# Optimization experiments

Hardware: AMD Instinct MI355X
Metric: run time of the kernel (lower is better)

## Reference

```python
import jax, jax.numpy as jnp
import numpy as np

NUM_REF = 20
LINE_SCORE_THRESH = 0.6
MIN_PLANE_AREA = 100
H, W, N_LINES = 480, 640, 100


def _sobel(x):
    # x: [B,1,H,W] -> [B,2,H,W]; standard Sobel edge conv (kx, ky), padding=1
    kx = jnp.array([[1., 0., -1.], [2., 0., -2.], [1., 0., -1.]], x.dtype)
    ky = jnp.array([[1., 2., 1.], [0., 0., 0.], [-1., -2., -1.]], x.dtype)
    k = jnp.stack([kx, ky])[:, None]  # [2,1,3,3]
    return jax.lax.conv_general_dilated(x, k, (1, 1), [(1, 1), (1, 1)],
                                         dimension_numbers=('NCHW', 'OIHW', 'NCHW'))


def setup_inputs() -> dict:
    key = jax.random.key(0)
    k1, k2, k3, k4, k5 = jax.random.split(key, 5)
    depth_pred = jax.random.normal(k1, (1, 1, H, W), jnp.float32)
    depth_gt = jax.random.uniform(k2, (1, 1, H, W), jnp.float32)
    line_pred = jax.random.uniform(k3, (1, N_LINES, 6), jnp.float32)
    line_score = jax.random.normal(k4, (1, N_LINES, 2), jnp.float32)
    valid_mask = jax.random.randint(k5, (1, 1, H, W), 0, 2) > 0
    return {"depth_pred": depth_pred, "depth_gt": depth_gt,
            "line_pred": line_pred, "line_score": line_score,
            "valid_mask": valid_mask}


def reference(depth_pred, depth_gt, line_pred, line_score, valid_mask):
    h, w = depth_pred.shape[-2:]
    # how many lines pass the softmax threshold -> number of planes actually used
    probs = jax.nn.softmax(line_score, axis=-1)
    num_kept = jnp.sum(probs[0, :, 0] > LINE_SCORE_THRESH)
    top_num = jnp.minimum(num_kept, NUM_REF)
    # top-k by raw class-0 logit (torch.topk is sorted, so top `top_num` = prefix)
    _, t_ids = jax.lax.top_k(line_score[0, :, 0], NUM_REF)
    chosen = line_pred[0][t_ids]  # [P,6]
    scale = jnp.array([w, h, w, h, w, h], jnp.float32)
    xy = jnp.round(chosen * scale).reshape(NUM_REF, 3, 2)  # [P,3,(x,y)]
    xy = jnp.stack([jnp.clip(xy[..., 0], 0, w - 1),
                    jnp.clip(xy[..., 1], 0, h - 1)], axis=-1)
    # Sobel normal map
    g = _sobel(depth_pred)              # [1,2,H,W]
    nx, ny = -g[0, 0], -g[0, 1]          # [H,W]
    valid = valid_mask[0, 0]             # [H,W] bool
    # vectorized point-in-triangle: cross-product sign test for all P planes
    px = jnp.arange(w, dtype=jnp.float32).reshape(1, 1, 1, w)
    py = jnp.arange(h, dtype=jnp.float32).reshape(1, 1, h, 1)
    nxt = xy[:, jnp.array([1, 2, 0])]
    ex = (nxt[..., 0] - xy[..., 0])[..., None, None]  # [P,3,1,1]
    ey = (nxt[..., 1] - xy[..., 1])[..., None, None]
    vx = xy[..., 0][..., None, None]
    vy = xy[..., 1][..., None, None]
    d = ex * (py - vy) - ey * (px - vx)               # [P,3,H,W]
    inside = jnp.all(d >= 0, axis=1) | jnp.all(d <= 0, axis=1)  # [P,H,W]
    m = inside & valid
    cnt = jnp.sum(m, axis=(1, 2)).astype(jnp.float32)  # [P]
    safe = jnp.maximum(cnt, 1.0)
    mf = m.astype(nx.dtype)
    mean_x = jnp.sum(mf * nx, axis=(1, 2)) / safe
    mean_y = jnp.sum(mf * ny, axis=(1, 2)) / safe
    var_x = jnp.sum(mf * (nx - mean_x[:, None, None]) ** 2, axis=(1, 2)) / safe
    var_y = jnp.sum(mf * (ny - mean_y[:, None, None]) ** 2, axis=(1, 2)) / safe
    include = (cnt >= MIN_PLANE_AREA) & (jnp.arange(NUM_REF) < top_num)
    total = jnp.maximum(jnp.sum(include), 1).astype(jnp.float32)
    loss_var = jnp.sum(jnp.where(include, var_x + var_y, 0.0)) / total
    return loss_var
```

## Files before the change

### kernel.cpp

```cpp
#include <hip/hip_runtime.h>
#include <math.h>

#define HH 480
#define WW 640
#define NL 100
#define NREF 20
#define RPB 2
#define NB (HH / RPB)


__global__ __launch_bounds__(256) void plane_main_kernel(
    const float* __restrict__ depth, const int* __restrict__ valid,
    const float* __restrict__ line_pred, const float* __restrict__ line_score,
    float* __restrict__ w) {
    __shared__ float ds[(RPB + 2) * WW];
    __shared__ int vsh[RPB * WW];
    __shared__ float s_sc[NL];
    __shared__ float s_vert[NREF][6];
    __shared__ float s_ae[RPB][NREF * 3];
    __shared__ float s_ey[NREF * 3];

    const int tid = threadIdx.x;
    const int base = blockIdx.x * RPB;

    if (tid < NL) s_sc[tid] = ((const float2*)line_score)[tid].x;

    for (int idx = tid; idx < (RPB + 2) * (WW / 4); idx += 256) {
        const int lr = idx / (WW / 4);
        const int c4 = idx - lr * (WW / 4);
        const int g = base - 1 + lr;
        float4 v = make_float4(0.f, 0.f, 0.f, 0.f);
        if ((unsigned)g < (unsigned)HH) v = ((const float4*)depth)[g * (WW / 4) + c4];
        ((float4*)ds)[idx] = v;
    }
    for (int idx = tid; idx < RPB * (WW / 4); idx += 256)
        ((int4*)vsh)[idx] = ((const int4*)valid)[base * (WW / 4) + idx];
    __syncthreads();

    if (tid < NL) {
        const float s0 = s_sc[tid];
        int rank = 0;
        for (int j = 0; j < NL; j++) {
            const float sj = s_sc[j];
            rank += ((sj > s0) || (sj == s0 && j < tid)) ? 1 : 0;
        }
        if (rank < NREF) {
            const float2 c01 = ((const float2*)line_pred)[3 * tid];
            const float2 c23 = ((const float2*)line_pred)[3 * tid + 1];
            const float2 c45 = ((const float2*)line_pred)[3 * tid + 2];
            s_vert[rank][0] = fminf(fmaxf(rintf(c01.x * (float)WW), 0.f), (float)(WW - 1));
            s_vert[rank][1] = fminf(fmaxf(rintf(c01.y * (float)HH), 0.f), (float)(HH - 1));
            s_vert[rank][2] = fminf(fmaxf(rintf(c23.x * (float)WW), 0.f), (float)(WW - 1));
            s_vert[rank][3] = fminf(fmaxf(rintf(c23.y * (float)HH), 0.f), (float)(HH - 1));
            s_vert[rank][4] = fminf(fmaxf(rintf(c45.x * (float)WW), 0.f), (float)(WW - 1));
            s_vert[rank][5] = fminf(fmaxf(rintf(c45.y * (float)HH), 0.f), (float)(HH - 1));
        }
    }
    __syncthreads();

    if (tid < NREF * 3) {
        const int t = tid / 3, e = tid - 3 * t, n = (e + 1) % 3;
        const float vx = s_vert[t][2 * e], vy = s_vert[t][2 * e + 1];
        const float ex = s_vert[t][2 * n] - vx, eyv = s_vert[t][2 * n + 1] - vy;
        s_ey[tid] = eyv;
        #pragma unroll
        for (int rr = 0; rr < RPB; rr++)
            s_ae[rr][tid] = fmaf(ex, (float)(base + rr) - vy, eyv * vx);
    }
    __syncthreads();

    const int wid = tid >> 6, lane = tid & 63;
    float eyr[5][3];
    #pragma unroll
    for (int i = 0; i < 5; i++)
        #pragma unroll
        for (int e = 0; e < 3; e++)
            eyr[i][e] = s_ey[(wid * 5 + i) * 3 + e];

    float acc[5][4];
    #pragma unroll
    for (int i = 0; i < 5; i++)
        #pragma unroll
        for (int q = 0; q < 4; q++) acc[i][q] = 0.f;

    #pragma unroll
    for (int rr = 0; rr < RPB; rr++) {
        float ae[5][3];
        #pragma unroll
        for (int i = 0; i < 5; i++)
            #pragma unroll
            for (int e = 0; e < 3; e++)
                ae[i][e] = s_ae[rr][(wid * 5 + i) * 3 + e];
        const float* rm = ds + rr * WW;
        const float* rc = ds + (rr + 1) * WW;
        const float* rp = ds + (rr + 2) * WW;
        const int* vrow = vsh + rr * WW;
        #pragma unroll
        for (int j = 0; j < 10; j++) {
            const int x = j * 64 + lane;
            const float px = (float)x;
            const float fl = (x > 0) ? 1.f : 0.f;
            const float fr = (x < WW - 1) ? 1.f : 0.f;
            const int xm = x - (x > 0), xp = x + (x < WW - 1);
            const float a00 = rm[xm] * fl, a01 = rm[x], a02 = rm[xp] * fr;
            const float a10 = rc[xm] * fl,               a12 = rc[xp] * fr;
            const float a20 = rp[xm] * fl, a21 = rp[x], a22 = rp[xp] * fr;
            const float gx = (a00 - a02) + 2.f * (a10 - a12) + (a20 - a22);
            const float gy = (a00 + 2.f * a01 + a02) - (a20 + 2.f * a21 + a22);
            const float nx = -gx, ny = -gy;
            const float s2 = nx * nx + ny * ny;
            const bool vm = (vrow[x] != 0);
            #pragma unroll
            for (int i = 0; i < 5; i++) {
                const float d0 = fmaf(-eyr[i][0], px, ae[i][0]);
                const float d1 = fmaf(-eyr[i][1], px, ae[i][1]);
                const float d2 = fmaf(-eyr[i][2], px, ae[i][2]);
                const float dmin = fminf(fminf(d0, d1), d2);
                const float dmax = fmaxf(fmaxf(d0, d1), d2);
                const bool m = ((dmin >= 0.f) | (dmax <= 0.f)) & vm;
                const float mf = m ? 1.f : 0.f;
                acc[i][0] += mf;
                acc[i][1] = fmaf(mf, nx, acc[i][1]);
                acc[i][2] = fmaf(mf, ny, acc[i][2]);
                acc[i][3] = fmaf(mf, s2, acc[i][3]);
            }
        }
    }

    #pragma unroll
    for (int off = 32; off > 0; off >>= 1)
        #pragma unroll
        for (int i = 0; i < 5; i++)
            #pragma unroll
            for (int q = 0; q < 4; q++)
                acc[i][q] += __shfl_down(acc[i][q], off);
    if (lane == 0) {
        #pragma unroll
        for (int i = 0; i < 5; i++)
            #pragma unroll
            for (int q = 0; q < 4; q++)
                w[((wid * 5 + i) * 4 + q) * NB + blockIdx.x] = acc[i][q];
    }
}

__global__ __launch_bounds__(128) void plane_finalize_kernel(
    const float* __restrict__ line_score, const float* __restrict__ w,
    float* __restrict__ out) {
    __shared__ float s_col[NREF * 4];
    __shared__ int s_cnt[2];
    const int tid = threadIdx.x;
    const int lane = tid & 63, wid = tid >> 6;

    int flag = 0;
    if (tid < NL) {
        const float2 sc = ((const float2*)line_score)[tid];
        const float p0 = 1.0f / (1.0f + expf(sc.y - sc.x));
        flag = (p0 > 0.6f) ? 1 : 0;
    }
    const unsigned long long b = __ballot(flag);
    if (lane == 0) s_cnt[wid] = __popcll(b);

    if (tid < NREF * 4) {
        const float4* col = (const float4*)(w + tid * NB);
        float4 s4 = make_float4(0.f, 0.f, 0.f, 0.f);
        #pragma unroll 4
        for (int p = 0; p < NB / 4; p++) {
            const float4 v = col[p];
            s4.x += v.x; s4.y += v.y; s4.z += v.z; s4.w += v.w;
        }
        s_col[tid] = (s4.x + s4.y) + (s4.z + s4.w);
    }
    __syncthreads();

    const int topnum = min(s_cnt[0] + s_cnt[1], NREF);
    float val = 0.f, inc = 0.f;
    if (tid < NREF) {
        const float c  = s_col[tid * 4 + 0];
        const float sx = s_col[tid * 4 + 1];
        const float sy = s_col[tid * 4 + 2];
        const float sq = s_col[tid * 4 + 3];
        const float safe = fmaxf(c, 1.f);
        const float mx = sx / safe, my = sy / safe;
        const float var = (sq - 2.f * mx * sx - 2.f * my * sy
                           + c * (mx * mx + my * my)) / safe;
        inc = ((c >= 100.f) && (tid < topnum)) ? 1.f : 0.f;
        val = inc * var;
    }
    if (tid < 64) {
        #pragma unroll
        for (int off = 32; off > 0; off >>= 1) {
            val += __shfl_down(val, off);
            inc += __shfl_down(inc, off);
        }
        if (tid == 0) out[0] = val / fmaxf(inc, 1.f);
    }
}

extern "C" void kernel_launch(void* const* d_in, const int* in_sizes, int n_in,
                              void* d_out, int out_size, void* d_ws, size_t ws_size,
                              hipStream_t stream) {
    const float* depth_pred = (const float*)d_in[0];
    const float* line_pred  = (const float*)d_in[2];
    const float* line_score = (const float*)d_in[3];
    const int*   valid_mask = (const int*)d_in[4];
    float* out = (float*)d_out;
    float* w = (float*)d_ws;

    plane_main_kernel<<<NB, 256, 0, stream>>>(depth_pred, valid_mask,
                                              line_pred, line_score, w);
    plane_finalize_kernel<<<1, 128, 0, stream>>>(line_score, w, out);
}
```

Baseline: 78.24 us.

## Fuse finalize into main kernel via last-block atomic ticket

```diff
diff --git a/kernel.cpp b/kernel.cpp
--- a/kernel.cpp
+++ b/kernel.cpp
@@ -9,16 +9,19 @@
 #define NB (HH / RPB)
 
 
-__global__ __launch_bounds__(256) void plane_main_kernel(
+__global__ __launch_bounds__(256) void plane_fused_kernel(
     const float* __restrict__ depth, const int* __restrict__ valid,
     const float* __restrict__ line_pred, const float* __restrict__ line_score,
-    float* __restrict__ w) {
+    float* __restrict__ w, float* __restrict__ out) {
     __shared__ float ds[(RPB + 2) * WW];
     __shared__ int vsh[RPB * WW];
     __shared__ float s_sc[NL];
     __shared__ float s_vert[NREF][6];
     __shared__ float s_ae[RPB][NREF * 3];
     __shared__ float s_ey[NREF * 3];
+    __shared__ float s_col[NREF * 4];
+    __shared__ int s_cnt[2];
+    __shared__ int s_last;
 
     const int tid = threadIdx.x;
     const int base = blockIdx.x * RPB;
@@ -134,22 +137,27 @@
             #pragma unroll
             for (int q = 0; q < 4; q++)
                 acc[i][q] += __shfl_down(acc[i][q], off);
+
     if (lane == 0) {
         #pragma unroll
         for (int i = 0; i < 5; i++)
             #pragma unroll
             for (int q = 0; q < 4; q++)
-                w[((wid * 5 + i) * 4 + q) * NB + blockIdx.x] = acc[i][q];
-    }
-}
-
-__global__ __launch_bounds__(128) void plane_finalize_kernel(
-    const float* __restrict__ line_score, const float* __restrict__ w,
-    float* __restrict__ out) {
-    __shared__ float s_col[NREF * 4];
-    __shared__ int s_cnt[2];
-    const int tid = threadIdx.x;
-    const int lane = tid & 63, wid = tid >> 6;
+                __hip_atomic_store(
+                    &w[((wid * 5 + i) * 4 + q) * NB + blockIdx.x], acc[i][q],
+                    __ATOMIC_RELAXED, __HIP_MEMORY_SCOPE_AGENT);
+    }
+    asm volatile("s_waitcnt vmcnt(0)" ::: "memory");
+    __syncthreads();
+
+    if (tid == 0) {
+        int* ticket = (int*)(w + NREF * 4 * NB);
+        const int t = __hip_atomic_fetch_add(ticket, 1, __ATOMIC_RELAXED,
+                                             __HIP_MEMORY_SCOPE_AGENT);
+        s_last = (((unsigned)t % (unsigned)NB) == (unsigned)(NB - 1)) ? 1 : 0;
+    }
+    __syncthreads();
+    if (!s_last) return;
 
     int flag = 0;
     if (tid < NL) {
@@ -158,17 +166,25 @@
         flag = (p0 > 0.6f) ? 1 : 0;
     }
     const unsigned long long b = __ballot(flag);
-    if (lane == 0) s_cnt[wid] = __popcll(b);
+    if (lane == 0 && wid < 2) s_cnt[wid] = __popcll(b);
 
     if (tid < NREF * 4) {
-        const float4* col = (const float4*)(w + tid * NB);
-        float4 s4 = make_float4(0.f, 0.f, 0.f, 0.f);
+        float* colp = w + tid * NB;
+        float sx0 = 0.f, sx1 = 0.f, sx2 = 0.f, sx3 = 0.f;
         #pragma unroll 4
         for (int p = 0; p < NB / 4; p++) {
-            const float4 v = col[p];
-            s4.x += v.x; s4.y += v.y; s4.z += v.z; s4.w += v.w;
-        }
-        s_col[tid] = (s4.x + s4.y) + (s4.z + s4.w);
+            const unsigned long long u0 = __hip_atomic_load(
+                (unsigned long long*)(colp + 4 * p),
+                __ATOMIC_RELAXED, __HIP_MEMORY_SCOPE_AGENT);
+            const unsigned long long u1 = __hip_atomic_load(
+                (unsigned long long*)(colp + 4 * p + 2),
+                __ATOMIC_RELAXED, __HIP_MEMORY_SCOPE_AGENT);
+            sx0 += __uint_as_float((unsigned)u0);
+            sx1 += __uint_as_float((unsigned)(u0 >> 32));
+            sx2 += __uint_as_float((unsigned)u1);
+            sx3 += __uint_as_float((unsigned)(u1 >> 32));
+        }
+        s_col[tid] = (sx0 + sx1) + (sx2 + sx3);
     }
     __syncthreads();
 
@@ -206,7 +222,6 @@
     float* out = (float*)d_out;
     float* w = (float*)d_ws;
 
-    plane_main_kernel<<<NB, 256, 0, stream>>>(depth_pred, valid_mask,
-                                              line_pred, line_score, w);
-    plane_finalize_kernel<<<1, 128, 0, stream>>>(line_score, w, out);
+    plane_fused_kernel<<<NB, 256, 0, stream>>>(depth_pred, valid_mask,
+                                               line_pred, line_score, w, out);
 }
```

Measured after the change: 81.15 us. 3.7% more time.
